# Optimization experiments

Hardware: AMD Instinct MI355X
Metric: run time of the kernel (lower is better)

The kernel has to match this reference:

```python
import jax, jax.numpy as jnp
import numpy as np

# Static grid / camera configuration (mirrors module __init__ defaults)
XB = [-50.0, 50.0, 0.5]
YB = [-50.0, 50.0, 0.5]
ZB = [-10.0, 10.0, 20.0]
DB = [4.0, 44.0, 0.5]
DOWN = 16
OGH, OGW = 384, 640
FH, FW = OGH // DOWN, OGW // DOWN  # 24, 40


def _precompute():
    """Replicates _create_frustum + _get_geometry with the default (identity)
    camera parameters. All results are static integer index structures."""
    dx = np.array([XB[2], YB[2], ZB[2]])
    bx = np.array([XB[0] + XB[2] / 2.0, YB[0] + YB[2] / 2.0, ZB[0] + ZB[2] / 2.0])
    nx = np.array([int((r[1] - r[0]) / r[2]) for r in (XB, YB, ZB)])  # [200,200,1]

    ds = np.arange(DB[0], DB[1], DB[2], dtype=np.float64)  # (80,)
    xs = np.linspace(0.0, OGW - 1, FW)
    ys = np.linspace(0.0, OGH - 1, FH)
    # frustum (D, fH, fW, 3) with last dim = (x_pix, y_pix, depth)
    f = np.stack(np.broadcast_arrays(xs[None, None, :], ys[None, :, None], ds[:, None, None]), -1)

    # default cam params: post_rot=I, post_trans=0, rots=I, trans=0
    K = np.array([[320.0, 0.0, 320.0], [0.0, 320.0, 180.0], [0.0, 0.0, 1.0]])
    pts = np.concatenate([f[..., :2] * f[..., 2:3], f[..., 2:3]], -1)
    pts = pts @ np.linalg.inv(K).T  # combine = rots @ inv(K) = inv(K)

    # voxelize; torch .long() truncates toward zero, replicate with np.trunc
    vox = np.trunc((pts - (bx - dx / 2.0)) / dx).astype(np.int64).reshape(-1, 3)
    B = 1
    pts4 = np.concatenate([vox, np.zeros((vox.shape[0], 1), dtype=np.int64)], 1)

    kept = ((vox[:, 0] >= 0) & (vox[:, 0] < nx[0]) &
            (vox[:, 1] >= 0) & (vox[:, 1] < nx[1]) &
            (vox[:, 2] >= 0) & (vox[:, 2] < nx[2]))
    idx_kept = np.nonzero(kept)[0]
    pk = pts4[kept]
    ranks = (pk[:, 0] * (nx[1] * nx[2] * B) + pk[:, 1] * (nx[2] * B)
             + pk[:, 2] * B + pk[:, 3])
    sorts = np.argsort(ranks, kind='stable')
    ranks = ranks[sorts]
    pk = pk[sorts]
    gather_idx = idx_kept[sorts]  # indices into the flat (B*D*H*W) point axis

    new_seg = np.concatenate([[0], (ranks[1:] != ranks[:-1]).astype(np.int64)])
    seg_ids = np.cumsum(new_seg)
    n_seg = int(seg_ids[-1]) + 1
    kept2 = np.ones(len(ranks), dtype=bool)
    kept2[:-1] = ranks[1:] != ranks[:-1]
    geom = pk[kept2]  # unique voxel coords (n_seg, 4) = (ix, iy, iz, b)
    return nx, gather_idx, seg_ids, n_seg, geom

_NX, _GIDX, _SEG, _NSEG, _GEOM = _precompute()


def setup_inputs() -> dict:
    key = jax.random.key(0)
    k1, k2 = jax.random.split(key)
    feat = jax.random.normal(k1, (1, 512, FH, FW), dtype=jnp.float32)
    depth = jax.random.uniform(k2, (1, 80, FH, FW), dtype=jnp.float32)
    return {"feat": feat, "depth": depth}


def reference(feat, depth):
    B, C, H, W = feat.shape
    # outer product over depth bins: (B, C, D, H, W)
    x = depth[:, None, ...] * feat[:, :, None, ...]
    x = jnp.transpose(x, (1, 0, 2, 3, 4)).reshape(C, -1)  # (C, B*D*H*W)

    # gather kept points in rank-sorted order (the x[:, sorts_t][:, :lens] step)
    xs = jnp.take(x, jnp.asarray(_GIDX), axis=1)  # (C, lens)

    # segmented sum over equal-rank runs (equivalent to the cumsum trick)
    seg = jax.ops.segment_sum(xs.T, jnp.asarray(_SEG), num_segments=_NSEG)  # (n_seg, C)

    # scatter into dense voxel grid (nx0, nx1, nx2, B, C); ranks are unique
    g = jnp.asarray(_GEOM)
    final = jnp.zeros((int(_NX[0]), int(_NX[1]), int(_NX[2]), B, C), dtype=feat.dtype)
    final = final.at[g[:, 0], g[:, 1], g[:, 2], g[:, 3]].set(seg)
    # (B, C, nx2, nx0, nx1) -> collapse z (nx2 == 1)
    return jnp.transpose(final, (3, 4, 2, 0, 1))[:, :, 0, :, :]
```

## Files before the change

kernel.cpp:

```cpp
#include <hip/hip_runtime.h>
#include <stdint.h>


#define NX0 200
#define NX1 200
#define NC 512
#define FH 24
#define FW 40
#define NRAY (FH * FW)
#define ND 12
#define BX0 80
#define BNX 40
#define BY0 88
#define BNY 26
#define NVB (BNX * BNY)
#define NPTS (NRAY * ND)

struct Tab {
    int      csr[NVB + 1];
    uint32_t ent[NPTS];
};

constexpr Tab build_tab() {
    Tab t{};
    int vox[NPTS] = {};
    for (int ray = 0; ray < NRAY; ++ray) {
        const int w = ray % FW, h = ray / FW;
        const double a = 1.0 / 320.0;
        const double u = (w == FW - 1) ? 639.0 : (double)w * (639.0 / 39.0);
        const double v = (h == FH - 1) ? 383.0 : (double)h * (383.0 / 23.0);
        for (int k = 0; k < ND; ++k) {
            const double d = 4.0 + 0.5 * (double)k;
            const double x = (u * d) * a - d;
            const double y = (v * d) * a - 0.5625 * d;
            const int ix = (int)((x + 50.0) * 2.0);
            const int iy = (int)((y + 50.0) * 2.0);
            vox[k * NRAY + ray] = (ix - BX0) * BNY + (iy - BY0);
        }
    }
    int cnt[NVB] = {};
    for (int i = 0; i < NPTS; ++i) ++cnt[vox[i]];
    t.csr[0] = 0;
    for (int lv = 0; lv < NVB; ++lv) t.csr[lv + 1] = t.csr[lv] + cnt[lv];
    int pos[NVB] = {};
    for (int lv = 0; lv < NVB; ++lv) pos[lv] = t.csr[lv];
    for (int i = 0; i < NPTS; ++i) {
        const int lv  = vox[i];
        const int ray = i % NRAY;
        t.ent[pos[lv]++] = (uint32_t)i | ((uint32_t)ray << 16);
    }
    return t;
}

__constant__ Tab c_tab = build_tab();

__global__ __launch_bounds__(256)
void lss_fuse(const float* __restrict__ feat, const float* __restrict__ depth,
              float* __restrict__ out) {
    __shared__ float s_dep[NPTS];
    __shared__ float s_feat[NRAY];
    const int c   = blockIdx.x;
    const int tid = threadIdx.x;

    const float4* d4 = (const float4*)depth;
    for (int i = tid; i < NPTS / 4; i += 256)
        ((float4*)s_dep)[i] = d4[i];
    if (tid < NRAY / 4)
        ((float4*)s_feat)[tid] = ((const float4*)(feat + c * NRAY))[tid];
    __syncthreads();

    float* oc = out + (size_t)c * (NX0 * NX1);
    for (int lv = tid; lv < NVB; lv += 256) {
        const int e0 = c_tab.csr[lv], e1 = c_tab.csr[lv + 1];
        float s = 0.0f;
        for (int e = e0; e < e1; ++e) {
            const uint32_t p = c_tab.ent[e];
            s += s_dep[p & 0xFFFFu] * s_feat[p >> 16];
        }
        const int ixo = lv / BNY;
        const int iyo = lv - ixo * BNY;
        oc[(BX0 + ixo) * NX1 + (BY0 + iyo)] = s;
    }
}

extern "C" void kernel_launch(void* const* d_in, const int* in_sizes, int n_in,
                              void* d_out, int out_size, void* d_ws, size_t ws_size,
                              hipStream_t stream) {
    const float* feat  = (const float*)d_in[0];
    const float* depth = (const float*)d_in[1];
    float* out = (float*)d_out;

    hipMemsetAsync(out, 0, (size_t)out_size * sizeof(float), stream);
    lss_fuse<<<NC, 256, 0, stream>>>(feat, depth, out);
}
```

Baseline: 114.5 us.

## Fuse output zero-fill into the kernel and store full rows with vector writes

Removes the separate memset and launches extra blocks that zero the parts of each channel plane outside the active voxel rows using nontemporal float4 stores. The main blocks stage their voxel sums in shared memory, then write the full 200-wide rows of the active x-range, padding zeros around the 26 active columns, as aligned vector stores. This avoids writing the output twice and avoids scattered scalar writes. The cost is a larger grid with a branch between block roles, plus an extra sync and shared buffer.

Result: no change. 116.5 us (+1.8%).

```diff
diff --git a/kernel.cpp b/kernel.cpp
--- a/kernel.cpp
+++ b/kernel.cpp
@@ -15,6 +15,9 @@
 #define BNY 26
 #define NVB (BNX * BNY)
 #define NPTS (NRAY * ND)
+#define PLANE (NX0 * NX1)
+
+typedef float f32x4 __attribute__((ext_vector_type(4)));
 
 struct Tab {
     int      csr[NVB + 1];
@@ -55,31 +58,57 @@
 __constant__ Tab c_tab = build_tab();
 
 __global__ __launch_bounds__(256)
-void lss_fuse(const float* __restrict__ feat, const float* __restrict__ depth,
-              float* __restrict__ out) {
-    __shared__ float s_dep[NPTS];
-    __shared__ float s_feat[NRAY];
-    const int c   = blockIdx.x;
+void lss_one(const float* __restrict__ feat, const float* __restrict__ depth,
+             float* __restrict__ out) {
+    const int b   = blockIdx.x;
     const int tid = threadIdx.x;
 
-    const float4* d4 = (const float4*)depth;
-    for (int i = tid; i < NPTS / 4; i += 256)
-        ((float4*)s_dep)[i] = d4[i];
-    if (tid < NRAY / 4)
-        ((float4*)s_feat)[tid] = ((const float4*)(feat + c * NRAY))[tid];
-    __syncthreads();
+    if (b < NC) {
+        __shared__ float s_dep[NPTS];
+        __shared__ float s_feat[NRAY];
+        __shared__ float s_act[NVB];
 
-    float* oc = out + (size_t)c * (NX0 * NX1);
-    for (int lv = tid; lv < NVB; lv += 256) {
-        const int e0 = c_tab.csr[lv], e1 = c_tab.csr[lv + 1];
-        float s = 0.0f;
-        for (int e = e0; e < e1; ++e) {
-            const uint32_t p = c_tab.ent[e];
-            s += s_dep[p & 0xFFFFu] * s_feat[p >> 16];
+        const int c = b;
+        const float4* d4 = (const float4*)depth;
+        for (int i = tid; i < NPTS / 4; i += 256)
+            ((float4*)s_dep)[i] = d4[i];
+        if (tid < NRAY / 4)
+            ((float4*)s_feat)[tid] = ((const float4*)(feat + c * NRAY))[tid];
+        __syncthreads();
+
+        for (int lv = tid; lv < NVB; lv += 256) {
+            const int e0 = c_tab.csr[lv], e1 = c_tab.csr[lv + 1];
+            float s = 0.0f;
+            for (int e = e0; e < e1; ++e) {
+                const uint32_t p = c_tab.ent[e];
+                s += s_dep[p & 0xFFFFu] * s_feat[p >> 16];
+            }
+            s_act[lv] = s;
         }
-        const int ixo = lv / BNY;
-        const int iyo = lv - ixo * BNY;
-        oc[(BX0 + ixo) * NX1 + (BY0 + iyo)] = s;
+        __syncthreads();
+
+        float* oc = out + (size_t)c * PLANE + BX0 * NX1;
+        for (int idx = tid; idx < BNX * 50; idx += 256) {
+            const int row = idx / 50;
+            const int q   = idx - row * 50;
+            f32x4 r = {0.f, 0.f, 0.f, 0.f};
+            const float* ar = s_act + row * BNY;
+#pragma unroll
+            for (int j = 0; j < 4; ++j) {
+                const int col = 4 * q + j;
+                if ((unsigned)(col - BY0) < BNY) r[j] = ar[col - BY0];
+            }
+            __builtin_nontemporal_store(r, (f32x4*)(oc + row * NX1 + 4 * q));
+        }
+    } else {
+        const int t   = b - NC;
+        const int c   = t >> 2;
+        const int q   = t & 3;
+        const int off = q * 8000 + ((q >= 2) ? 8000 : 0);
+        float* base = out + (size_t)c * PLANE + off;
+        const f32x4 z = {0.f, 0.f, 0.f, 0.f};
+        for (int i = tid; i < 2000; i += 256)
+            __builtin_nontemporal_store(z, (f32x4*)(base + 4 * i));
     }
 }
 
@@ -90,6 +119,5 @@
     const float* depth = (const float*)d_in[1];
     float* out = (float*)d_out;
 
-    hipMemsetAsync(out, 0, (size_t)out_size * sizeof(float), stream);
-    lss_fuse<<<NC, 256, 0, stream>>>(feat, depth, out);
+    lss_one<<<NC + 4 * NC, 256, 0, stream>>>(feat, depth, out);
 }
```
